# Performance work log

Hardware: AMD Instinct MI355X
Metric: run time of the kernel (lower is better)

The kernel has to match this reference:

```python
import jax, jax.numpy as jnp
import numpy as np
from jax import lax

NUM_SAMPLE = 1024   # init_kwargs: num_sample
RADIUS = 0.1        # init_kwargs: ball_query_radius (compared against SQUARED distance, as in original)


def setup_inputs() -> dict:
    key = jax.random.key(0)
    x = jax.random.normal(key, (4, 32768, 131), dtype=jnp.float32)  # [B, N, 3+C]
    return {"x": x}


def _fps_single(pts, num_sample):
    # pts: [N, 3]. Faithful to source: seed index is overwritten at i=0, so the
    # only effect of the seed is the first distance update; we use a
    # deterministic seed of 0 instead of python random.randint.
    n = pts.shape[0]

    def step(carry, _):
        closest, sel = carry
        d = jnp.sum((pts[sel] - pts) ** 2, axis=-1)      # [N]
        closest = jnp.minimum(d, closest)
        sel = jnp.argmax(closest).astype(jnp.int32)
        return (closest, sel), sel

    init = (jnp.full((n,), jnp.inf, dtype=jnp.float32), jnp.int32(0))
    _, idx = lax.scan(step, init, None, length=num_sample)
    return idx  # [M] int32


def _ball_query_counts(pts, idx, radius):
    # pts: [N,3], idx: [M]. Original builds variable-length index lists; the
    # jit-static equivalent is the membership mask d2 <= radius. We return the
    # per-centroid member counts (summary of the mask).
    cent = pts[idx]                                                 # [M, 3]
    d2 = jnp.sum((cent[:, None, :] - pts[None, :, :]) ** 2, axis=-1)  # [M, N]
    return jnp.sum(d2 <= radius, axis=-1).astype(jnp.int32)          # [M]


def reference(x):
    pts = x[:, :, :3]                                    # [B, N, 3]
    idx = jax.vmap(lambda p: _fps_single(p, NUM_SAMPLE))(pts)            # [B, M]
    counts = jax.vmap(lambda p, i: _ball_query_counts(p, i, RADIUS))(pts, idx)  # [B, M]
    # Original forward returns x unchanged; idx/counts are returned as well so
    # the FPS + ball-query compute is observable and not dead-code-eliminated.
    return (x, idx, counts)
```

## Files before the change

kernel.cpp:

```cpp
#include <hip/hip_runtime.h>
#include <math.h>

#define B 4
#define N 32768
#define D 131
#define S 1024
#define RAD2 0.1f
#define G 16
#define TPB 256
#define PPT 8
#define NFPS (B * G)
#define COPY_BLOCKS 192

__global__ void pack_kernel(const float* __restrict__ x, float* __restrict__ ws) {
    int i = blockIdx.x * blockDim.x + threadIdx.x;
    if (i < B * N) {
        const float* __restrict__ s = x + (size_t)i * D;
        float a = s[0], bb = s[1], c = s[2];
        ws[i]             = a;
        ws[B * N + i]     = bb;
        ws[2 * B * N + i] = c;
        float4* w4 = (float4*)(ws + (size_t)3 * B * N);
        w4[i] = make_float4(a, bb, c, 0.0f);
    }
}

__launch_bounds__(TPB)
__global__ void fps_copy_kernel(const float* __restrict__ x,
                                const float* __restrict__ ws,
                                unsigned long long* __restrict__ gslot,
                                float* __restrict__ out_idx,
                                int* __restrict__ idx_int,
                                float* __restrict__ out_x) {
    if (blockIdx.x >= NFPS) {
        const size_t total4 = (size_t)B * N * D / 4;
        const float4* __restrict__ src = (const float4*)x;
        float4* __restrict__ dst = (float4*)out_x;
        for (size_t i = (size_t)(blockIdx.x - NFPS) * TPB + threadIdx.x; i < total4;
             i += (size_t)COPY_BLOCKS * TPB)
            dst[i] = src[i];
        return;
    }

    const int b = blockIdx.x >> 4;
    const int g = blockIdx.x & 15;
    const int t = threadIdx.x;
    const int lane = t & 63;
    const int w = t >> 6;

    __shared__ unsigned long long s_wk[2][4];

    const float* __restrict__ px = ws + (size_t)b * N;
    const float* __restrict__ py = ws + (size_t)(B + b) * N;
    const float* __restrict__ pz = ws + (size_t)(2 * B + b) * N;
    const float4* __restrict__ p4 = (const float4*)(ws + (size_t)3 * B * N) + (size_t)b * N;
    unsigned long long* __restrict__ slots = gslot + (size_t)b * 2 * G;

    const int base = g * (N / G);
    float lx[PPT], ly[PPT], lz[PPT], lcl[PPT];
    #pragma unroll
    for (int i = 0; i < PPT / 2; ++i) {
        int p = base + 2 * t + 2 * TPB * i;
        float2 vx = *(const float2*)&px[p];
        float2 vy = *(const float2*)&py[p];
        float2 vz = *(const float2*)&pz[p];
        lx[2*i] = vx.x; lx[2*i+1] = vx.y;
        ly[2*i] = vy.x; ly[2*i+1] = vy.y;
        lz[2*i] = vz.x; lz[2*i+1] = vz.y;
        lcl[2*i] = INFINITY; lcl[2*i+1] = INFINITY;
    }

    float4 c4 = p4[0];

    for (int s = 0; s < S; ++s) {
        const float cx = c4.x, cy = c4.y, cz = c4.z;

        float best = -INFINITY;
        int   bidx = 0;
        #pragma unroll
        for (int i = 0; i < PPT / 2; ++i) {
            const int p = base + 2 * t + 2 * TPB * i;
            {
                float dx = __fsub_rn(cx, lx[2*i]);
                float dy = __fsub_rn(cy, ly[2*i]);
                float dz = __fsub_rn(cz, lz[2*i]);
                float d2 = __fadd_rn(__fadd_rn(__fmul_rn(dx, dx), __fmul_rn(dy, dy)),
                                     __fmul_rn(dz, dz));
                float c = fminf(lcl[2*i], d2);
                lcl[2*i] = c;
                if (c > best) { best = c; bidx = p; }
            }
            {
                float dx = __fsub_rn(cx, lx[2*i+1]);
                float dy = __fsub_rn(cy, ly[2*i+1]);
                float dz = __fsub_rn(cz, lz[2*i+1]);
                float d2 = __fadd_rn(__fadd_rn(__fmul_rn(dx, dx), __fmul_rn(dy, dy)),
                                     __fmul_rn(dz, dz));
                float c = fminf(lcl[2*i+1], d2);
                lcl[2*i+1] = c;
                if (c > best) { best = c; bidx = p + 1; }
            }
        }

        unsigned hi  = __float_as_uint(best);
        unsigned lo2 = (unsigned)(32767 - bidx);

        #define FPS_COMBINE(OHI, OLO) \
            { unsigned _oh = (OHI), _ol = (OLO); \
              if (_oh > hi || (_oh == hi && _ol > lo2)) { hi = _oh; lo2 = _ol; } }
        { unsigned a = (unsigned)__builtin_amdgcn_update_dpp(0, (int)hi, 0xB1, 0xf, 0xf, true);
          unsigned c2 = (unsigned)__builtin_amdgcn_update_dpp(0, (int)lo2, 0xB1, 0xf, 0xf, true);
          FPS_COMBINE(a, c2); }
        { unsigned a = (unsigned)__builtin_amdgcn_update_dpp(0, (int)hi, 0x4E, 0xf, 0xf, true);
          unsigned c2 = (unsigned)__builtin_amdgcn_update_dpp(0, (int)lo2, 0x4E, 0xf, 0xf, true);
          FPS_COMBINE(a, c2); }
        { unsigned a = (unsigned)__builtin_amdgcn_update_dpp(0, (int)hi, 0x141, 0xf, 0xf, true);
          unsigned c2 = (unsigned)__builtin_amdgcn_update_dpp(0, (int)lo2, 0x141, 0xf, 0xf, true);
          FPS_COMBINE(a, c2); }
        { unsigned a = (unsigned)__builtin_amdgcn_update_dpp(0, (int)hi, 0x140, 0xf, 0xf, true);
          unsigned c2 = (unsigned)__builtin_amdgcn_update_dpp(0, (int)lo2, 0x140, 0xf, 0xf, true);
          FPS_COMBINE(a, c2); }
        { unsigned a = (unsigned)__builtin_amdgcn_ds_swizzle((int)hi, 0x401F);
          unsigned c2 = (unsigned)__builtin_amdgcn_ds_swizzle((int)lo2, 0x401F);
          FPS_COMBINE(a, c2); }
        { unsigned a = (unsigned)__shfl_xor((int)hi, 32, 64);
          unsigned c2 = (unsigned)__shfl_xor((int)lo2, 32, 64);
          FPS_COMBINE(a, c2); }
        #undef FPS_COMBINE

        const int buf = s & 1;
        const unsigned tag = (unsigned)(s + 1);
        const unsigned long long mykey = ((unsigned long long)hi << 32) |
                                         ((unsigned long long)lo2 << 17) | tag;
        if (lane == 0) s_wk[buf][w] = mykey;
        __syncthreads();

        unsigned long long bk = s_wk[buf][0];
        #pragma unroll
        for (int j = 1; j < 4; ++j) { unsigned long long v = s_wk[buf][j]; if (v > bk) bk = v; }
        if (t == 0)
            __hip_atomic_store(&slots[buf * G + g], bk, __ATOMIC_RELAXED,
                               __HIP_MEMORY_SCOPE_AGENT);

        unsigned long long kk;
        unsigned long long* myslot = &slots[buf * G + (lane & 15)];
        do {
            kk = __hip_atomic_load(myslot, __ATOMIC_RELAXED, __HIP_MEMORY_SCOPE_AGENT);
        } while (__any((unsigned)(kk & 0x7FFull) != tag));

        #pragma unroll
        for (int off = 1; off < 16; off <<= 1) {
            unsigned long long o = (unsigned long long)__shfl_xor((long long)kk, off, 64);
            if (o > kk) kk = o;
        }
        int sel = 32767 - (int)((kk >> 17) & 0x7FFF);
        sel = __builtin_amdgcn_readfirstlane(sel);

        if (g == 0 && t == 0) {
            out_idx[(size_t)b * S + s] = (float)sel;
            idx_int[b * S + s] = sel;
        }
        c4 = p4[sel];
    }
}

__launch_bounds__(256)
__global__ void ballq_kernel(const float* __restrict__ ws,
                             const int* __restrict__ idx_int,
                             float* __restrict__ out_counts) {
    __shared__ int s_part[4];
    const int b = blockIdx.x >> 10;
    const int j = blockIdx.x & 1023;
    const int t = threadIdx.x;
    const float* __restrict__ px = ws + (size_t)b * N;
    const float* __restrict__ py = ws + (size_t)(B + b) * N;
    const float* __restrict__ pz = ws + (size_t)(2 * B + b) * N;

    const int ci = idx_int[b * S + j];
    const float cx = px[ci], cy = py[ci], cz = pz[ci];

    int cnt = 0;
    #pragma unroll 4
    for (int p = t; p < N; p += 256) {
        float dx = __fsub_rn(cx, px[p]);
        float dy = __fsub_rn(cy, py[p]);
        float dz = __fsub_rn(cz, pz[p]);
        float d2 = __fadd_rn(__fadd_rn(__fmul_rn(dx, dx), __fmul_rn(dy, dy)),
                             __fmul_rn(dz, dz));
        cnt += (d2 <= RAD2) ? 1 : 0;
    }
    #pragma unroll
    for (int off = 1; off < 64; off <<= 1)
        cnt += __shfl_xor(cnt, off, 64);
    if ((t & 63) == 0) s_part[t >> 6] = cnt;
    __syncthreads();
    if (t == 0)
        out_counts[b * S + j] = (float)(s_part[0] + s_part[1] + s_part[2] + s_part[3]);
}

extern "C" void kernel_launch(void* const* d_in, const int* in_sizes, int n_in,
                              void* d_out, int out_size, void* d_ws, size_t ws_size,
                              hipStream_t stream) {
    const float* x = (const float*)d_in[0];
    float* out = (float*)d_out;
    float* ws = (float*)d_ws;
    int* idx_int = (int*)(ws + (size_t)7 * B * N);
    unsigned long long* gslot = (unsigned long long*)(idx_int + B * S);

    float* out_x      = out;
    float* out_idx    = out + (size_t)B * N * D;
    float* out_counts = out_idx + (size_t)B * S;

    hipMemsetAsync(gslot, 0, (size_t)B * 2 * G * sizeof(unsigned long long), stream);

    hipLaunchKernelGGL(pack_kernel, dim3((B * N + 255) / 256), dim3(256), 0, stream, x, ws);
    hipLaunchKernelGGL(fps_copy_kernel, dim3(NFPS + COPY_BLOCKS), dim3(TPB), 0, stream,
                       x, ws, gslot, out_idx, idx_int, out_x);
    hipLaunchKernelGGL(ballq_kernel, dim3(B * S), dim3(256), 0, stream, ws, idx_int, out_counts);
}
```

Measured before the change: 2.353 ms.

## Poll global slots from one wave and broadcast centroid via LDS flag

Only wave 0 now polls the cross-block global slots. Each lane speculatively loads the candidate centroid coordinates for its slot before the reduction finishes, and the winning lane's coordinates are shuffled out. The other waves spin on an LDS tag and read the broadcast coordinates, which removes redundant global polling and the dependent p4[sel] load from the per-iteration critical path. The cost is an LDS spin-wait and extra speculative gathers, and the flag protocol depends on a threadfence ordering the LDS writes.

```diff
diff --git a/kernel.cpp b/kernel.cpp
--- a/kernel.cpp
+++ b/kernel.cpp
@@ -49,6 +49,8 @@
     const int w = t >> 6;
 
     __shared__ unsigned long long s_wk[2][4];
+    __shared__ float s_bc[3];
+    __shared__ unsigned s_tag;
 
     const float* __restrict__ px = ws + (size_t)b * N;
     const float* __restrict__ py = ws + (size_t)(B + b) * N;
@@ -69,12 +71,13 @@
         lz[2*i] = vz.x; lz[2*i+1] = vz.y;
         lcl[2*i] = INFINITY; lcl[2*i+1] = INFINITY;
     }
-
-    float4 c4 = p4[0];
+    if (t == 0) s_tag = 0;
+    __syncthreads();
+
+    float4 cq = p4[0];
+    float cx = cq.x, cy = cq.y, cz = cq.z;
 
     for (int s = 0; s < S; ++s) {
-        const float cx = c4.x, cy = c4.y, cz = c4.z;
-
         float best = -INFINITY;
         int   bidx = 0;
         #pragma unroll
@@ -104,7 +107,6 @@
 
         unsigned hi  = __float_as_uint(best);
         unsigned lo2 = (unsigned)(32767 - bidx);
-
         #define FPS_COMBINE(OHI, OLO) \
             { unsigned _oh = (OHI), _ol = (OLO); \
               if (_oh > hi || (_oh == hi && _ol > lo2)) { hi = _oh; lo2 = _ol; } }
@@ -135,32 +137,52 @@
         if (lane == 0) s_wk[buf][w] = mykey;
         __syncthreads();
 
-        unsigned long long bk = s_wk[buf][0];
-        #pragma unroll
-        for (int j = 1; j < 4; ++j) { unsigned long long v = s_wk[buf][j]; if (v > bk) bk = v; }
-        if (t == 0)
-            __hip_atomic_store(&slots[buf * G + g], bk, __ATOMIC_RELAXED,
-                               __HIP_MEMORY_SCOPE_AGENT);
-
-        unsigned long long kk;
-        unsigned long long* myslot = &slots[buf * G + (lane & 15)];
-        do {
-            kk = __hip_atomic_load(myslot, __ATOMIC_RELAXED, __HIP_MEMORY_SCOPE_AGENT);
-        } while (__any((unsigned)(kk & 0x7FFull) != tag));
-
-        #pragma unroll
-        for (int off = 1; off < 16; off <<= 1) {
-            unsigned long long o = (unsigned long long)__shfl_xor((long long)kk, off, 64);
-            if (o > kk) kk = o;
+        if (w == 0) {
+            unsigned long long bk = s_wk[buf][0];
+            #pragma unroll
+            for (int j = 1; j < 4; ++j) { unsigned long long v = s_wk[buf][j]; if (v > bk) bk = v; }
+            if (lane == 0)
+                __hip_atomic_store(&slots[buf * G + g], bk, __ATOMIC_RELAXED,
+                                   __HIP_MEMORY_SCOPE_AGENT);
+
+            unsigned long long kk;
+            unsigned long long* myslot = &slots[buf * G + (lane & 15)];
+            do {
+                kk = __hip_atomic_load(myslot, __ATOMIC_RELAXED, __HIP_MEMORY_SCOPE_AGENT);
+            } while (__any((unsigned)(kk & 0x7FFull) != tag));
+
+            const unsigned long long kko = kk;
+            const int idxc = 32767 - (int)((kko >> 17) & 0x7FFF);
+            const float4 cand = p4[idxc];
+
+            #pragma unroll
+            for (int off = 1; off < 16; off <<= 1) {
+                unsigned long long o = (unsigned long long)__shfl_xor((long long)kk, off, 64);
+                if (o > kk) kk = o;
+            }
+            unsigned long long mask = __ballot(kko == kk);
+            int src = (int)(__ffsll((unsigned long long)mask) - 1);
+            cx = __shfl(cand.x, src, 64);
+            cy = __shfl(cand.y, src, 64);
+            cz = __shfl(cand.z, src, 64);
+
+            if (lane == 0) {
+                s_bc[0] = cx; s_bc[1] = cy; s_bc[2] = cz;
+                __threadfence_block();
+                __hip_atomic_store(&s_tag, tag, __ATOMIC_RELAXED,
+                                   __HIP_MEMORY_SCOPE_WORKGROUP);
+                if (g == 0) {
+                    int sel = 32767 - (int)((kk >> 17) & 0x7FFF);
+                    out_idx[(size_t)b * S + s] = (float)sel;
+                    idx_int[b * S + s] = sel;
+                }
+            }
+        } else {
+            while (__hip_atomic_load(&s_tag, __ATOMIC_RELAXED,
+                                     __HIP_MEMORY_SCOPE_WORKGROUP) != tag) {}
+            __threadfence_block();
+            cx = s_bc[0]; cy = s_bc[1]; cz = s_bc[2];
         }
-        int sel = 32767 - (int)((kk >> 17) & 0x7FFF);
-        sel = __builtin_amdgcn_readfirstlane(sel);
-
-        if (g == 0 && t == 0) {
-            out_idx[(size_t)b * S + s] = (float)sel;
-            idx_int[b * S + s] = sel;
-        }
-        c4 = p4[sel];
     }
 }
 
```

Measured after the change: 1.938 ms, median of 2. -17.6%, faster.
